# Performance work log

Hardware: AMD Instinct MI355X
Metric: run time of the kernel (lower is better)

The kernel has to match this reference:

```python
import jax, jax.numpy as jnp
import numpy as np

K = 16          # neighbors per query (args.k)
EPS_NORM = 1e-5  # LayerNorm / BatchNorm eps (torch default)


def _knn_edges(xyz, B, n):
    # batch-aware kNN: equal-sized batches, edges never cross batch boundary
    x = xyz.reshape(B, n, 3)
    d2 = jnp.sum((x[:, :, None, :] - x[:, None, :, :]) ** 2, -1)   # [B,n,n]
    _, idx = jax.lax.top_k(-d2, K)                                 # [B,n,K] local neighbor ids
    col = (idx + (jnp.arange(B) * n)[:, None, None]).reshape(-1)   # source (neighbor) [E]
    row = jnp.repeat(jnp.arange(B * n), K)                         # target (query)    [E]
    return row, col


def _forward(support_xyz, batch_index, features, lang_features, mask_flattened,
             W1, b1, ln_g, ln_b, W2, b2,
             Wl1, bl1, bn_g, bn_b, Wl2, bl2,
             Wr1, br1, Wr2, br2, row, col):
    N = support_xyz.shape[0]
    B, L, Fl = lang_features.shape
    # feat_encoder: Linear -> LayerNorm -> ReLU -> Linear
    h = features @ W1 + b1
    mu = h.mean(-1, keepdims=True)
    var = ((h - mu) ** 2).mean(-1, keepdims=True)
    h = (h - mu) / jnp.sqrt(var + EPS_NORM) * ln_g + ln_b
    feats = jax.nn.relu(h) @ W2 + b2                               # [N,F]
    # lang_encoder: Linear -> BatchNorm1d (batch statistics) -> ReLU -> Linear
    hl = lang_features.reshape(B * L, Fl) @ Wl1 + bl1
    mul = hl.mean(0)
    varl = ((hl - mul) ** 2).mean(0)
    hl = (hl - mul) / jnp.sqrt(varl + EPS_NORM) * bn_g + bn_b
    lang = (jax.nn.relu(hl) @ Wl2 + bl2).reshape(B, L, -1)         # [B,L,F]
    lang_flat = lang[batch_index]                                  # [N,L,F]
    # per-point / per-token attention logits
    atten = jnp.einsum('nf,nlf->nl', feats, lang_flat)             # [N,L]
    # segment softmax over incoming kNN edges (CenterOp max / add)
    attenmax = jax.ops.segment_max(atten[col], row, num_segments=N, indices_are_sorted=True)
    a = jnp.exp(atten[col] - attenmax[row])                        # [E,L]
    attensum = jax.ops.segment_sum(a, row, num_segments=N, indices_are_sorted=True)
    # CenterConv message
    att = a / attensum[row] * mask_flattened[row]                  # [E,L]
    att = att / (att.sum(-1, keepdims=True) + 1e-7)
    ctx = jnp.einsum('el,elf->ef', att, lang_flat[col])            # [E,F] attended lang feat
    xi, xj = support_xyz[row], support_xyz[col]
    d = xi - xj
    nrm = jnp.sqrt(jnp.sum(d * d, -1, keepdims=True) + 1e-12)
    ew = jnp.concatenate([xi, xj, d, nrm], -1)                     # [E,10]
    ew = jax.nn.relu(ew @ Wr1 + br1) @ Wr2 + br2                   # [E,F] rel_encoder
    msg = feats[col] * ctx * ew                                    # [E,F]
    rel = jax.ops.segment_sum(msg, row, num_segments=N, indices_are_sorted=True)
    return feats + rel


def setup_inputs() -> dict:
    key = jax.random.key(0)
    ks = jax.random.split(key, 12)
    B, n, L = 4, 1024, 16
    N = B * n
    Fv, Fl, F = 256, 768, 128
    def w(k, shp, fan):
        return jax.random.normal(k, shp, jnp.float32) / np.sqrt(fan).astype(np.float32)
    mask = (jax.random.uniform(ks[3], (N, L)) < 0.8).astype(jnp.float32).at[:, 0].set(1.0)
    return {
        'support_xyz': jax.random.normal(ks[0], (N, 3), jnp.float32),
        'batch_index': jnp.repeat(jnp.arange(B), n),
        'features': jax.random.normal(ks[1], (N, Fv), jnp.float32),
        'lang_features': jax.random.normal(ks[2], (B, L, Fl), jnp.float32),
        'mask_flattened': mask,
        'W1': w(ks[4], (Fv, F), Fv), 'b1': jnp.zeros(F, jnp.float32),
        'ln_g': jnp.ones(F, jnp.float32), 'ln_b': jnp.zeros(F, jnp.float32),
        'W2': w(ks[5], (F, F), F), 'b2': jnp.zeros(F, jnp.float32),
        'Wl1': w(ks[6], (Fl, F), Fl), 'bl1': jnp.zeros(F, jnp.float32),
        'bn_g': jnp.ones(F, jnp.float32), 'bn_b': jnp.zeros(F, jnp.float32),
        'Wl2': w(ks[7], (F, F), F), 'bl2': jnp.zeros(F, jnp.float32),
        'Wr1': w(ks[8], (10, 64), 10), 'br1': jnp.zeros(64, jnp.float32),
        'Wr2': w(ks[9], (64, F), 64), 'br2': jnp.zeros(F, jnp.float32),
    }


def reference(support_xyz, batch_index, features, lang_features, mask_flattened,
              W1, b1, ln_g, ln_b, W2, b2,
              Wl1, bl1, bn_g, bn_b, Wl2, bl2,
              Wr1, br1, Wr2, br2):
    B = lang_features.shape[0]
    n = support_xyz.shape[0] // B
    row, col = _knn_edges(support_xyz, B, n)
    return _forward(support_xyz, batch_index, features, lang_features, mask_flattened,
                    W1, b1, ln_g, ln_b, W2, b2,
                    Wl1, bl1, bn_g, bn_b, Wl2, bl2,
                    Wr1, br1, Wr2, br2, row, col)
```

## Files before the change

kernel.cpp:

```cpp
#include <hip/hip_runtime.h>

typedef unsigned long long u64;
typedef short short8 __attribute__((ext_vector_type(8)));
typedef short short4v __attribute__((ext_vector_type(4)));
typedef float f32x4 __attribute__((ext_vector_type(4)));

#define N_PTS   4096
#define B_SZ    4
#define N_PER_B 1024
#define L_TOK   16
#define FV      256
#define FL      768
#define FDIM    128
#define KNN     16
#define RH      64

#define FINS 264
#define RBS  136
#define FBS  132

__device__ __forceinline__ short f2bf(float f) {
    unsigned int x = __float_as_uint(f);
    unsigned int r = (x + 0x7fffu + ((x >> 16) & 1u)) >> 16;
    return (short)r;
}
__device__ __forceinline__ float bf2f(short s) {
    return __uint_as_float(((unsigned int)(unsigned short)s) << 16);
}
__device__ __forceinline__ int mbcnt64(u64 m) {
    return __builtin_amdgcn_mbcnt_hi((unsigned)(m >> 32),
                                     __builtin_amdgcn_mbcnt_lo((unsigned)m, 0));
}

__global__ __launch_bounds__(256, 2) void kA_kernel(const float* __restrict__ xyz,
                                                 const float* __restrict__ lf,
                                                 const float* __restrict__ Wl1,
                                                 const float* __restrict__ bl1,
                                                 const float* __restrict__ Wr2,
                                                 const float* __restrict__ W1,
                                                 const float* __restrict__ W2,
                                                 int* __restrict__ knn,
                                                 float* __restrict__ hl,
                                                 short* __restrict__ wr2t,
                                                 short* __restrict__ w1t_hi,
                                                 short* __restrict__ w1t_lo,
                                                 short* __restrict__ w2t_hi,
                                                 short* __restrict__ w2t_lo) {
    __shared__ float smem[1024];
    int b = blockIdx.x, t = threadIdx.x;

    if (b < 1024) {
        int lane = t & 63;
        int q = b * 4 + (t >> 6);
        int base = (q >> 10) << 10;
        float qx = xyz[q * 3 + 0];
        float qy = xyz[q * 3 + 1];
        float qz = xyz[q * 3 + 2];
        unsigned keys[16];
#pragma unroll
        for (int m = 0; m < 16; m++) {
            int j = base + lane + (m << 6);
            float dx = qx - xyz[j * 3 + 0];
            float dy = qy - xyz[j * 3 + 1];
            float dz = qz - xyz[j * 3 + 2];
            float d2 = __fadd_rn(__fadd_rn(__fmul_rn(dx, dx), __fmul_rn(dy, dy)),
                                 __fmul_rn(dz, dz));
            keys[m] = __float_as_uint(d2);
        }
        unsigned prefix = 0;
        int need = 16;
#pragma unroll
        for (int bit = 30; bit >= 0; --bit) {
            unsigned lim = 1u << bit;
            int c = 0;
#pragma unroll
            for (int m = 0; m < 16; m++)
                c += __popcll(__ballot((keys[m] ^ prefix) < lim));
            if (c < need) {
                need -= c;
                prefix |= lim;
            }
        }
        int pos = 0;
#pragma unroll
        for (int m = 0; m < 16; m++) {
            bool less = keys[m] < prefix;
            bool eqv  = (keys[m] == prefix);
            u64 em = __ballot(eqv);
            bool take_eq = false;
            if (need > 0) {
                int ec = __popcll(em);
                if (ec <= need) {
                    take_eq = eqv;
                    need -= ec;
                } else {
                    take_eq = eqv && (mbcnt64(em) < need);
                    need = 0;
                }
            }
            bool sel = less || take_eq;
            u64 sm = __ballot(sel);
            if (sel) {
                int my = pos + mbcnt64(sm);
                knn[q * KNN + my] = base + lane + (m << 6);
            }
            pos += __popcll(sm);
        }
    } else if (b < 1088) {
        int r = b - 1024;
        float* lrow = smem;
        float* part = smem + 768;
        for (int k = t; k < FL; k += 256) lrow[k] = lf[r * FL + k];
        __syncthreads();
        int c = t & 127, kh = t >> 7;
        float acc = (kh == 0) ? bl1[c] : 0.f;
        int k0 = kh * 384;
#pragma unroll 8
        for (int k = k0; k < k0 + 384; k++) acc += lrow[k] * Wl1[k * FDIM + c];
        part[kh * FDIM + c] = acc;
        __syncthreads();
        if (kh == 0) hl[r * FDIM + c] = part[c] + part[FDIM + c];
    } else if (b == 1088) {
        for (int p = t; p < RH * FDIM; p += 256) {
            int c = p >> 6, k = p & 63;
            wr2t[c * RH + k] = f2bf(Wr2[k * FDIM + c]);
        }
    } else if (b == 1089) {
        for (int p = t; p < FDIM * FDIM; p += 256) {
            int k = p >> 7, c = p & 127;
            float v = W2[p];
            short h = f2bf(v);
            w2t_hi[c * FDIM + k] = h;
            w2t_lo[c * FDIM + k] = f2bf(v - bf2f(h));
        }
    } else {
        int kbase = (b - 1090) * 128;
        for (int p = t; p < 128 * FDIM; p += 256) {
            int k = kbase + (p >> 7), c = p & 127;
            float v = W1[k * FDIM + c];
            short h = f2bf(v);
            w1t_hi[c * FV + k] = h;
            w1t_lo[c * FV + k] = f2bf(v - bf2f(h));
        }
    }
}

__global__ __launch_bounds__(128) void lang2_kernel(const float* __restrict__ hl,
                                                    const float* __restrict__ bn_g,
                                                    const float* __restrict__ bn_b,
                                                    const float* __restrict__ Wl2,
                                                    const float* __restrict__ bl2,
                                                    float* __restrict__ lang,
                                                    short* __restrict__ langT) {
    __shared__ float rl4[4][FDIM];
    int t = threadIdx.x;
    int r0 = blockIdx.x * 4;
    float s = 0.f, s2 = 0.f;
#pragma unroll 8
    for (int r = 0; r < 64; r++) {
        float v = hl[r * FDIM + t];
        s += v; s2 += v * v;
    }
    float mu = s * (1.f / 64.f);
    float var = s2 * (1.f / 64.f) - mu * mu;
    float rs = rsqrtf(var + 1e-5f);
    float g = bn_g[t], bb = bn_b[t];
#pragma unroll
    for (int p = 0; p < 4; p++)
        rl4[p][t] = fmaxf((hl[(r0 + p) * FDIM + t] - mu) * rs * g + bb, 0.f);
    __syncthreads();
    float bv = bl2[t];
    float a[4] = {bv, bv, bv, bv};
#pragma unroll 8
    for (int k = 0; k < FDIM; k++) {
        float w = Wl2[k * FDIM + t];
        a[0] += rl4[0][k] * w;
        a[1] += rl4[1][k] * w;
        a[2] += rl4[2][k] * w;
        a[3] += rl4[3][k] * w;
    }
#pragma unroll
    for (int p = 0; p < 4; p++) {
        int r = r0 + p;
        lang[r * FDIM + t] = a[p];
        langT[((r >> 4) * FDIM + t) * L_TOK + (r & 15)] = f2bf(a[p]);
    }
}

__global__ __launch_bounds__(256) void feat_kernel(const float* __restrict__ features,
                                                   const float* __restrict__ b1,
                                                   const float* __restrict__ ln_g,
                                                   const float* __restrict__ ln_b,
                                                   const float* __restrict__ b2,
                                                   const short* __restrict__ w1t_hi,
                                                   const short* __restrict__ w1t_lo,
                                                   const short* __restrict__ w2t_hi,
                                                   const short* __restrict__ w2t_lo,
                                                   const float* __restrict__ lang,
                                                   float* __restrict__ feats,
                                                   float* __restrict__ atten) {
    __shared__ short fin_hi[16 * FINS], fin_lo[16 * FINS];
    __shared__ short rb_hi[16 * RBS], rb_lo[16 * RBS];
    __shared__ float fbuf[16 * FBS];
    __shared__ float red_s[4 * 16], red_q[4 * 16];
    int t = threadIdx.x;
    int w = t >> 6, lane = t & 63, quad = lane >> 4, e16 = lane & 15;
    int i0 = blockIdx.x * 16;

    {
        const float4* src = (const float4*)(features + i0 * FV);
#pragma unroll
        for (int v = 0; v < 4; v++) {
            int flat = t + 256 * v;
            float4 x = src[flat];
            int p = flat >> 6, k = (flat & 63) * 4;
            short4v hi, lo;
            hi[0] = f2bf(x.x); lo[0] = f2bf(x.x - bf2f(hi[0]));
            hi[1] = f2bf(x.y); lo[1] = f2bf(x.y - bf2f(hi[1]));
            hi[2] = f2bf(x.z); lo[2] = f2bf(x.z - bf2f(hi[2]));
            hi[3] = f2bf(x.w); lo[3] = f2bf(x.w - bf2f(hi[3]));
            *(short4v*)&fin_hi[p * FINS + k] = hi;
            *(short4v*)&fin_lo[p * FINS + k] = lo;
        }
    }
    __syncthreads();

    int c0 = 32 * w + e16, c1 = c0 + 16;

    f32x4 acc0 = {0.f, 0.f, 0.f, 0.f}, acc1 = {0.f, 0.f, 0.f, 0.f};
#pragma unroll
    for (int s = 0; s < 8; s++) {
        int ko = s * 32 + quad * 8;
        short8 Ah = *(const short8*)&fin_hi[e16 * FINS + ko];
        short8 Al = *(const short8*)&fin_lo[e16 * FINS + ko];
        short8 B0h = *(const short8*)&w1t_hi[c0 * FV + ko];
        short8 B0l = *(const short8*)&w1t_lo[c0 * FV + ko];
        short8 B1h = *(const short8*)&w1t_hi[c1 * FV + ko];
        short8 B1l = *(const short8*)&w1t_lo[c1 * FV + ko];
        acc0 = __builtin_amdgcn_mfma_f32_16x16x32_bf16(Ah, B0h, acc0, 0, 0, 0);
        acc0 = __builtin_amdgcn_mfma_f32_16x16x32_bf16(Ah, B0l, acc0, 0, 0, 0);
        acc0 = __builtin_amdgcn_mfma_f32_16x16x32_bf16(Al, B0h, acc0, 0, 0, 0);
        acc1 = __builtin_amdgcn_mfma_f32_16x16x32_bf16(Ah, B1h, acc1, 0, 0, 0);
        acc1 = __builtin_amdgcn_mfma_f32_16x16x32_bf16(Ah, B1l, acc1, 0, 0, 0);
        acc1 = __builtin_amdgcn_mfma_f32_16x16x32_bf16(Al, B1h, acc1, 0, 0, 0);
    }
    float b1c0 = b1[c0], b1c1 = b1[c1];
    float h0[4], h1[4], sp[4], qp[4];
#pragma unroll
    for (int r = 0; r < 4; r++) {
        h0[r] = acc0[r] + b1c0;
        h1[r] = acc1[r] + b1c1;
        sp[r] = h0[r] + h1[r];
        qp[r] = h0[r] * h0[r] + h1[r] * h1[r];
    }
#pragma unroll
    for (int off = 1; off < 16; off <<= 1) {
#pragma unroll
        for (int r = 0; r < 4; r++) {
            sp[r] += __shfl_xor(sp[r], off, 16);
            qp[r] += __shfl_xor(qp[r], off, 16);
        }
    }
    if (e16 == 0) {
#pragma unroll
        for (int r = 0; r < 4; r++) {
            red_s[w * 16 + quad * 4 + r] = sp[r];
            red_q[w * 16 + quad * 4 + r] = qp[r];
        }
    }
    __syncthreads();
    float g0 = ln_g[c0], g1 = ln_g[c1], be0 = ln_b[c0], be1 = ln_b[c1];
#pragma unroll
    for (int r = 0; r < 4; r++) {
        int p = quad * 4 + r;
        float S = red_s[p] + red_s[16 + p] + red_s[32 + p] + red_s[48 + p];
        float Q = red_q[p] + red_q[16 + p] + red_q[32 + p] + red_q[48 + p];
        float mu = S * (1.f / 128.f);
        float var = Q * (1.f / 128.f) - mu * mu;
        float rs = rsqrtf(var + 1e-5f);
        float r0 = fmaxf((h0[r] - mu) * rs * g0 + be0, 0.f);
        float r1 = fmaxf((h1[r] - mu) * rs * g1 + be1, 0.f);
        short hh;
        hh = f2bf(r0); rb_hi[p * RBS + c0] = hh; rb_lo[p * RBS + c0] = f2bf(r0 - bf2f(hh));
        hh = f2bf(r1); rb_hi[p * RBS + c1] = hh; rb_lo[p * RBS + c1] = f2bf(r1 - bf2f(hh));
    }
    __syncthreads();

    f32x4 o0 = {0.f, 0.f, 0.f, 0.f}, o1 = {0.f, 0.f, 0.f, 0.f};
#pragma unroll
    for (int s = 0; s < 4; s++) {
        int ko = s * 32 + quad * 8;
        short8 Ah = *(const short8*)&rb_hi[e16 * RBS + ko];
        short8 Al = *(const short8*)&rb_lo[e16 * RBS + ko];
        short8 B0h = *(const short8*)&w2t_hi[c0 * FDIM + ko];
        short8 B0l = *(const short8*)&w2t_lo[c0 * FDIM + ko];
        short8 B1h = *(const short8*)&w2t_hi[c1 * FDIM + ko];
        short8 B1l = *(const short8*)&w2t_lo[c1 * FDIM + ko];
        o0 = __builtin_amdgcn_mfma_f32_16x16x32_bf16(Ah, B0h, o0, 0, 0, 0);
        o0 = __builtin_amdgcn_mfma_f32_16x16x32_bf16(Ah, B0l, o0, 0, 0, 0);
        o0 = __builtin_amdgcn_mfma_f32_16x16x32_bf16(Al, B0h, o0, 0, 0, 0);
        o1 = __builtin_amdgcn_mfma_f32_16x16x32_bf16(Ah, B1h, o1, 0, 0, 0);
        o1 = __builtin_amdgcn_mfma_f32_16x16x32_bf16(Ah, B1l, o1, 0, 0, 0);
        o1 = __builtin_amdgcn_mfma_f32_16x16x32_bf16(Al, B1h, o1, 0, 0, 0);
    }
    float b20 = b2[c0], b21 = b2[c1];
#pragma unroll
    for (int r = 0; r < 4; r++) {
        int p = quad * 4 + r;
        float f0 = o0[r] + b20, f1 = o1[r] + b21;
        feats[(i0 + p) * FDIM + c0] = f0;
        feats[(i0 + p) * FDIM + c1] = f1;
        fbuf[p * FBS + c0] = f0;
        fbuf[p * FBS + c1] = f1;
    }
    __syncthreads();

    int pp = t >> 4, l = t & 15;
    int bi = i0 >> 10;
    const float4* lr = (const float4*)(lang + (bi * L_TOK + l) * FDIM);
    float acc = 0.f;
#pragma unroll
    for (int k = 0; k < FDIM / 4; k++) {
        float4 x = lr[k];
        float4 y = *(const float4*)&fbuf[pp * FBS + 4 * k];
        acc += x.x * y.x + x.y * y.y + x.z * y.z + x.w * y.w;
    }
    atten[(i0 + pp) * L_TOK + l] = acc;
}

__global__ __launch_bounds__(256) void edge_kernel(const float* __restrict__ xyz,
                                                   const float* __restrict__ mask,
                                                   const float* __restrict__ Wr1,
                                                   const float* __restrict__ br1,
                                                   const short* __restrict__ wr2t,
                                                   const float* __restrict__ br2,
                                                   const int* __restrict__ knn,
                                                   const short* __restrict__ langT,
                                                   const float* __restrict__ feats,
                                                   const float* __restrict__ atten,
                                                   float* __restrict__ out) {
    int lane = threadIdx.x & 63;
    int wid  = threadIdx.x >> 6;
    int i    = blockIdx.x * 4 + wid;
    int bi   = i >> 10;
    int quad = lane >> 4;
    int e16  = lane & 15;

    int idxe = knn[i * KNN + e16];

    float sat[8];
    if (quad < 2) {
        const float4* ap = (const float4*)(atten + idxe * L_TOK + quad * 8);
        float4 a0 = ap[0], a1 = ap[1];
        sat[0] = a0.x; sat[1] = a0.y; sat[2] = a0.z; sat[3] = a0.w;
        sat[4] = a1.x; sat[5] = a1.y; sat[6] = a1.z; sat[7] = a1.w;
    } else {
#pragma unroll
        for (int j = 0; j < 8; j++) sat[j] = 0.f;
    }

    float mx[8];
#pragma unroll
    for (int j = 0; j < 8; j++) mx[j] = sat[j];
#pragma unroll
    for (int off = 1; off < 16; off <<= 1) {
#pragma unroll
        for (int j = 0; j < 8; j++) mx[j] = fmaxf(mx[j], __shfl_xor(mx[j], off, 16));
    }
    float ex[8], sm[8];
#pragma unroll
    for (int j = 0; j < 8; j++) { ex[j] = __expf(sat[j] - mx[j]); sm[j] = ex[j]; }
#pragma unroll
    for (int off = 1; off < 16; off <<= 1) {
#pragma unroll
        for (int j = 0; j < 8; j++) sm[j] += __shfl_xor(sm[j], off, 16);
    }
    float st[8];
    if (quad < 2) {
        const float4* mp = (const float4*)(mask + i * L_TOK + quad * 8);
        float4 m0 = mp[0], m1 = mp[1];
        float mv[8] = {m0.x, m0.y, m0.z, m0.w, m1.x, m1.y, m1.z, m1.w};
#pragma unroll
        for (int j = 0; j < 8; j++) st[j] = ex[j] * (mv[j] / sm[j]);
    } else {
#pragma unroll
        for (int j = 0; j < 8; j++) st[j] = 0.f;
    }
    float s = st[0] + st[1] + st[2] + st[3] + st[4] + st[5] + st[6] + st[7];
    s += __shfl_xor(s, 16, 64);
    s += __shfl_xor(s, 32, 64);
    float inv2 = 1.f / (s + 1e-7f);
    short8 sattA;
#pragma unroll
    for (int j = 0; j < 8; j++) sattA[j] = f2bf(st[j] * inv2);

    float xi0 = xyz[i * 3 + 0], xi1 = xyz[i * 3 + 1], xi2 = xyz[i * 3 + 2];
    float xj0 = xyz[idxe * 3 + 0], xj1 = xyz[idxe * 3 + 1], xj2 = xyz[idxe * 3 + 2];
    float d0 = xi0 - xj0, d1 = xi1 - xj1, d2v = xi2 - xj2;
    float nr = sqrtf(d0 * d0 + d1 * d1 + d2v * d2v + 1e-12f);
    float ein[10] = {xi0, xi1, xi2, xj0, xj1, xj2, d0, d1, d2v, nr};
    short8 hidA[2];
#pragma unroll
    for (int sstep = 0; sstep < 2; sstep++) {
        int k0 = sstep * 32 + quad * 8;
        float h[8];
        const float4* bp = (const float4*)(br1 + k0);
        float4 b0 = bp[0], b1v = bp[1];
        h[0] = b0.x; h[1] = b0.y; h[2] = b0.z; h[3] = b0.w;
        h[4] = b1v.x; h[5] = b1v.y; h[6] = b1v.z; h[7] = b1v.w;
#pragma unroll
        for (int m = 0; m < 10; m++) {
            const float4* wp = (const float4*)(Wr1 + m * RH + k0);
            float4 w0 = wp[0], w1 = wp[1];
            float em = ein[m];
            h[0] += em * w0.x; h[1] += em * w0.y; h[2] += em * w0.z; h[3] += em * w0.w;
            h[4] += em * w1.x; h[5] += em * w1.y; h[6] += em * w1.z; h[7] += em * w1.w;
        }
#pragma unroll
        for (int j = 0; j < 8; j++) hidA[sstep][j] = f2bf(fmaxf(h[j], 0.f));
    }

    int idxr[4];
#pragma unroll
    for (int r = 0; r < 4; r++) idxr[r] = knn[i * KNN + quad * 4 + r];

#pragma unroll 2
    for (int tile = 0; tile < 8; tile++) {
        int cc = tile * 16 + e16;
        const short8* w2p = (const short8*)(wr2t + cc * RH);
        f32x4 accew = {0.f, 0.f, 0.f, 0.f};
        accew = __builtin_amdgcn_mfma_f32_16x16x32_bf16(hidA[0], w2p[quad],     accew, 0, 0, 0);
        accew = __builtin_amdgcn_mfma_f32_16x16x32_bf16(hidA[1], w2p[4 + quad], accew, 0, 0, 0);
        short8 lsB;
        if (quad < 2) {
            lsB = ((const short8*)(langT + (bi * FDIM + cc) * L_TOK))[quad];
        } else {
#pragma unroll
            for (int j = 0; j < 8; j++) lsB[j] = 0;
        }
        f32x4 accctx = {0.f, 0.f, 0.f, 0.f};
        accctx = __builtin_amdgcn_mfma_f32_16x16x32_bf16(sattA, lsB, accctx, 0, 0, 0);

        float br2c = br2[cc];
        float msum = 0.f;
#pragma unroll
        for (int r = 0; r < 4; r++) {
            float fj = feats[idxr[r] * FDIM + cc];
            msum += fj * accctx[r] * (accew[r] + br2c);
        }
        msum += __shfl_xor(msum, 16, 64);
        msum += __shfl_xor(msum, 32, 64);
        if (lane < 16)
            out[i * FDIM + cc] = feats[i * FDIM + cc] + msum;
    }
}

extern "C" void kernel_launch(void* const* d_in, const int* in_sizes, int n_in,
                              void* d_out, int out_size, void* d_ws, size_t ws_size,
                              hipStream_t stream) {
    const float* xyz   = (const float*)d_in[0];
    const float* features = (const float*)d_in[2];
    const float* lang_f   = (const float*)d_in[3];
    const float* mask     = (const float*)d_in[4];
    const float* W1   = (const float*)d_in[5];
    const float* b1   = (const float*)d_in[6];
    const float* ln_g = (const float*)d_in[7];
    const float* ln_b = (const float*)d_in[8];
    const float* W2   = (const float*)d_in[9];
    const float* b2   = (const float*)d_in[10];
    const float* Wl1  = (const float*)d_in[11];
    const float* bl1  = (const float*)d_in[12];
    const float* bn_g = (const float*)d_in[13];
    const float* bn_b = (const float*)d_in[14];
    const float* Wl2  = (const float*)d_in[15];
    const float* bl2  = (const float*)d_in[16];
    const float* Wr1  = (const float*)d_in[17];
    const float* br1  = (const float*)d_in[18];
    const float* Wr2  = (const float*)d_in[19];
    const float* br2  = (const float*)d_in[20];

    float* ws_feats = (float*)d_ws;
    float* ws_atten = ws_feats + N_PTS * FDIM;
    float* ws_lang  = ws_atten + N_PTS * L_TOK;
    float* ws_hl    = ws_lang + B_SZ * L_TOK * FDIM;
    int*   ws_knn   = (int*)(ws_hl + 64 * FDIM);
    short* ws_wr2t  = (short*)(ws_knn + N_PTS * KNN);
    short* ws_langT = ws_wr2t + FDIM * RH;
    short* ws_w1t_hi = ws_langT + B_SZ * FDIM * L_TOK;
    short* ws_w1t_lo = ws_w1t_hi + FDIM * FV;
    short* ws_w2t_hi = ws_w1t_lo + FDIM * FV;
    short* ws_w2t_lo = ws_w2t_hi + FDIM * FDIM;

    kA_kernel<<<1092, 256, 0, stream>>>(xyz, lang_f, Wl1, bl1, Wr2, W1, W2,
                                        ws_knn, ws_hl, ws_wr2t,
                                        ws_w1t_hi, ws_w1t_lo, ws_w2t_hi, ws_w2t_lo);
    lang2_kernel<<<16, 128, 0, stream>>>(ws_hl, bn_g, bn_b, Wl2, bl2,
                                         ws_lang, ws_langT);
    feat_kernel<<<N_PTS / 16, 256, 0, stream>>>(features, b1, ln_g, ln_b, b2,
                                                ws_w1t_hi, ws_w1t_lo,
                                                ws_w2t_hi, ws_w2t_lo,
                                                ws_lang, ws_feats, ws_atten);
    edge_kernel<<<N_PTS / 4, 256, 0, stream>>>(xyz, mask, Wr1, br1, ws_wr2t, br2,
                                               ws_knn, ws_langT, ws_feats, ws_atten,
                                               (float*)d_out);
}
```

Baseline: 170.5 us.

## Split kNN into own kernel with LDS-staged points and pruned radix select

Moves the kNN selection out of the combined prologue kernel into a dedicated kernel. The kernel stages the batch's 1024 points in shared memory and skips radix bits that are constant across all candidates, found with a wave-wide AND/OR reduction. It also counts with per-lane sums plus shuffles instead of 16 ballots per bit, and exits early once the count matches. The cost is an extra kernel launch, and the weight-prep work now runs serially after kNN instead of in the same grid.

```diff
diff --git a/kernel.cpp b/kernel.cpp
--- a/kernel.cpp
+++ b/kernel.cpp
@@ -32,14 +32,90 @@
                                      __builtin_amdgcn_mbcnt_lo((unsigned)m, 0));
 }
 
-__global__ __launch_bounds__(256, 2) void kA_kernel(const float* __restrict__ xyz,
-                                                 const float* __restrict__ lf,
+__global__ __launch_bounds__(256) void knn_kernel(const float* __restrict__ xyz,
+                                                  int* __restrict__ knn) {
+    __shared__ float sx[1024], sy[1024], sz[1024];
+    int t = threadIdx.x, b = blockIdx.x;
+    int base = (b >> 8) << 10;
+#pragma unroll
+    for (int p0 = 0; p0 < 4; p0++) {
+        int p = t + p0 * 256;
+        sx[p] = xyz[(base + p) * 3 + 0];
+        sy[p] = xyz[(base + p) * 3 + 1];
+        sz[p] = xyz[(base + p) * 3 + 2];
+    }
+    __syncthreads();
+    int lane = t & 63, w = t >> 6;
+    int q = b * 4 + w;
+    int ql = q & 1023;
+    float qx = sx[ql], qy = sy[ql], qz = sz[ql];
+    unsigned keys[16];
+#pragma unroll
+    for (int m = 0; m < 16; m++) {
+        int j = lane + (m << 6);
+        float dx = qx - sx[j], dy = qy - sy[j], dz = qz - sz[j];
+        float d2 = __fadd_rn(__fadd_rn(__fmul_rn(dx, dx), __fmul_rn(dy, dy)),
+                             __fmul_rn(dz, dz));
+        keys[m] = __float_as_uint(d2);
+    }
+    unsigned A = keys[0], O = keys[0];
+#pragma unroll
+    for (int m = 1; m < 16; m++) { A &= keys[m]; O |= keys[m]; }
+#pragma unroll
+    for (int off = 1; off < 64; off <<= 1) {
+        A &= (unsigned)__shfl_xor((int)A, off, 64);
+        O |= (unsigned)__shfl_xor((int)O, off, 64);
+    }
+    unsigned OS    = (unsigned)__builtin_amdgcn_readfirstlane((int)O);
+    unsigned diffS = (unsigned)__builtin_amdgcn_readfirstlane((int)(A ^ O));
+    unsigned prefix = 0;
+    int need = 16;
+    for (int bit = 30; bit >= 0; --bit) {
+        unsigned lim = 1u << bit;
+        if (!((diffS >> bit) & 1)) {
+            prefix |= (OS & lim);
+            continue;
+        }
+        unsigned cnt = 0;
+#pragma unroll
+        for (int m = 0; m < 16; m++)
+            cnt += ((keys[m] ^ prefix) < lim) ? 1u : 0u;
+#pragma unroll
+        for (int off = 1; off < 64; off <<= 1)
+            cnt += (unsigned)__shfl_xor((int)cnt, off, 64);
+        int c = __builtin_amdgcn_readfirstlane((int)cnt);
+        if (c == need) { prefix |= lim; need = 0; break; }
+        if (c < need) { need -= c; prefix |= lim; }
+    }
+    int pos = 0;
+#pragma unroll
+    for (int m = 0; m < 16; m++) {
+        unsigned key = keys[m];
+        bool less = key < prefix;
+        bool take_eq = false;
+        if (need > 0) {
+            bool eqv = (key == prefix);
+            u64 em = __ballot(eqv);
+            int ec = __popcll(em);
+            if (ec <= need) { take_eq = eqv; need -= ec; }
+            else { take_eq = eqv && (mbcnt64(em) < need); need = 0; }
+        }
+        bool sel = less || take_eq;
+        u64 sm = __ballot(sel);
+        if (sel) {
+            int my = pos + mbcnt64(sm);
+            knn[q * KNN + my] = base + lane + (m << 6);
+        }
+        pos += __popcll(sm);
+    }
+}
+
+__global__ __launch_bounds__(256) void kA_rest_kernel(const float* __restrict__ lf,
                                                  const float* __restrict__ Wl1,
                                                  const float* __restrict__ bl1,
                                                  const float* __restrict__ Wr2,
                                                  const float* __restrict__ W1,
                                                  const float* __restrict__ W2,
-                                                 int* __restrict__ knn,
                                                  float* __restrict__ hl,
                                                  short* __restrict__ wr2t,
                                                  short* __restrict__ w1t_hi,
@@ -48,66 +124,8 @@
                                                  short* __restrict__ w2t_lo) {
     __shared__ float smem[1024];
     int b = blockIdx.x, t = threadIdx.x;
-
-    if (b < 1024) {
-        int lane = t & 63;
-        int q = b * 4 + (t >> 6);
-        int base = (q >> 10) << 10;
-        float qx = xyz[q * 3 + 0];
-        float qy = xyz[q * 3 + 1];
-        float qz = xyz[q * 3 + 2];
-        unsigned keys[16];
-#pragma unroll
-        for (int m = 0; m < 16; m++) {
-            int j = base + lane + (m << 6);
-            float dx = qx - xyz[j * 3 + 0];
-            float dy = qy - xyz[j * 3 + 1];
-            float dz = qz - xyz[j * 3 + 2];
-            float d2 = __fadd_rn(__fadd_rn(__fmul_rn(dx, dx), __fmul_rn(dy, dy)),
-                                 __fmul_rn(dz, dz));
-            keys[m] = __float_as_uint(d2);
-        }
-        unsigned prefix = 0;
-        int need = 16;
-#pragma unroll
-        for (int bit = 30; bit >= 0; --bit) {
-            unsigned lim = 1u << bit;
-            int c = 0;
-#pragma unroll
-            for (int m = 0; m < 16; m++)
-                c += __popcll(__ballot((keys[m] ^ prefix) < lim));
-            if (c < need) {
-                need -= c;
-                prefix |= lim;
-            }
-        }
-        int pos = 0;
-#pragma unroll
-        for (int m = 0; m < 16; m++) {
-            bool less = keys[m] < prefix;
-            bool eqv  = (keys[m] == prefix);
-            u64 em = __ballot(eqv);
-            bool take_eq = false;
-            if (need > 0) {
-                int ec = __popcll(em);
-                if (ec <= need) {
-                    take_eq = eqv;
-                    need -= ec;
-                } else {
-                    take_eq = eqv && (mbcnt64(em) < need);
-                    need = 0;
-                }
-            }
-            bool sel = less || take_eq;
-            u64 sm = __ballot(sel);
-            if (sel) {
-                int my = pos + mbcnt64(sm);
-                knn[q * KNN + my] = base + lane + (m << 6);
-            }
-            pos += __popcll(sm);
-        }
-    } else if (b < 1088) {
-        int r = b - 1024;
+    if (b < 64) {
+        int r = b;
         float* lrow = smem;
         float* part = smem + 768;
         for (int k = t; k < FL; k += 256) lrow[k] = lf[r * FL + k];
@@ -120,12 +138,12 @@
         part[kh * FDIM + c] = acc;
         __syncthreads();
         if (kh == 0) hl[r * FDIM + c] = part[c] + part[FDIM + c];
-    } else if (b == 1088) {
+    } else if (b == 64) {
         for (int p = t; p < RH * FDIM; p += 256) {
             int c = p >> 6, k = p & 63;
             wr2t[c * RH + k] = f2bf(Wr2[k * FDIM + c]);
         }
-    } else if (b == 1089) {
+    } else if (b == 65) {
         for (int p = t; p < FDIM * FDIM; p += 256) {
             int k = p >> 7, c = p & 127;
             float v = W2[p];
@@ -134,7 +152,7 @@
             w2t_lo[c * FDIM + k] = f2bf(v - bf2f(h));
         }
     } else {
-        int kbase = (b - 1090) * 128;
+        int kbase = (b - 66) * 128;
         for (int p = t; p < 128 * FDIM; p += 256) {
             int k = kbase + (p >> 7), c = p & 127;
             float v = W1[k * FDIM + c];
@@ -491,9 +509,10 @@
     short* ws_w2t_hi = ws_w1t_lo + FDIM * FV;
     short* ws_w2t_lo = ws_w2t_hi + FDIM * FDIM;
 
-    kA_kernel<<<1092, 256, 0, stream>>>(xyz, lang_f, Wl1, bl1, Wr2, W1, W2,
-                                        ws_knn, ws_hl, ws_wr2t,
-                                        ws_w1t_hi, ws_w1t_lo, ws_w2t_hi, ws_w2t_lo);
+    knn_kernel<<<1024, 256, 0, stream>>>(xyz, ws_knn);
+    kA_rest_kernel<<<68, 256, 0, stream>>>(lang_f, Wl1, bl1, Wr2, W1, W2,
+                                           ws_hl, ws_wr2t,
+                                           ws_w1t_hi, ws_w1t_lo, ws_w2t_hi, ws_w2t_lo);
     lang2_kernel<<<16, 128, 0, stream>>>(ws_hl, bn_g, bn_b, Wl2, bl2,
                                          ws_lang, ws_langT);
     feat_kernel<<<N_PTS / 16, 256, 0, stream>>>(features, b1, ln_g, ln_b, b2,
```

Result: slower. 185.3 us (+8.7%).
